# Kernel optimization log

Hardware: AMD Instinct MI355X
Metric: run time of the kernel (lower is better)

The kernel has to match this reference:

```python
import jax, jax.numpy as jnp
import numpy as np

N = 100_000      # total nodes across batch of graphs
E = 1_600_000    # total directed edges
D = 128          # input feature dim
H = 128          # hidden dim
OUT = 10         # output classes
B = 500          # number of graphs (200 nodes each)
L_MID = 3        # GIN layers after the first (num_layers-2)


def setup_inputs() -> dict:
    key = jax.random.key(0)
    ks = jax.random.split(key, 24)
    s = np.float32(1.0 / np.sqrt(H))
    f32 = jnp.float32
    inp = {
        'node_features': jax.random.normal(ks[0], (N, D), f32),
        'edge_src': jax.random.randint(ks[1], (E,), 0, N, jnp.int32),
        'edge_dst': jax.random.randint(ks[2], (E,), 0, N, jnp.int32),
        'graph_ids': (jnp.arange(N) // (N // B)).astype(jnp.int32),
        # GIN eps per layer (torch init: zeros)
        'eps': jnp.zeros((4,), f32),
        # pre MLP (input layer): Linear(D,H) -> BN -> ReLU -> Linear(H,H), then pre_batchnorm
        'pre_W1': jax.random.normal(ks[3], (D, H), f32) * s,
        'pre_b1': jnp.zeros((H,), f32),
        'pre_g1': jnp.ones((H,), f32),
        'pre_bt1': jnp.zeros((H,), f32),
        'pre_W2': jax.random.normal(ks[4], (H, H), f32) * s,
        'pre_b2': jnp.zeros((H,), f32),
        'pre_gout': jnp.ones((H,), f32),
        'pre_btout': jnp.zeros((H,), f32),
        # middle GIN layers (stacked over L_MID)
        'mlp_W1': jax.random.normal(ks[5], (L_MID, H, H), f32) * s,
        'mlp_b1': jnp.zeros((L_MID, H), f32),
        'mlp_g1': jnp.ones((L_MID, H), f32),
        'mlp_bt1': jnp.zeros((L_MID, H), f32),
        'mlp_W2': jax.random.normal(ks[6], (L_MID, H, H), f32) * s,
        'mlp_b2': jnp.zeros((L_MID, H), f32),
        'bn_g': jnp.ones((L_MID, H), f32),
        'bn_bt': jnp.zeros((L_MID, H), f32),
        # per-layer prediction heads
        'pred_W0': jax.random.normal(ks[7], (D, OUT), f32) * s,
        'pred_b0': jnp.zeros((OUT,), f32),
        'pred_W': jax.random.normal(ks[8], (4, H, OUT), f32) * s,
        'pred_b': jnp.zeros((4, OUT), f32),
    }
    return inp


def _mlp_bn(x, W1, b1, g1, bt1, W2, b2, go, bo):
    # MLP(num_mlp_layers=2): Linear -> BN(eval) -> ReLU -> Linear, then outer BN(eval) -> ReLU
    h = jax.nn.relu(g1 * (x @ W1 + b1) + bt1)
    h = h @ W2 + b2
    return jax.nn.relu(go * h + bo)


def reference(node_features, edge_src, edge_dst, graph_ids, eps,
              pre_W1, pre_b1, pre_g1, pre_bt1, pre_W2, pre_b2, pre_gout, pre_btout,
              mlp_W1, mlp_b1, mlp_g1, mlp_bt1, mlp_W2, mlp_b2, bn_g, bn_bt,
              pred_W0, pred_b0, pred_W, pred_b):
    def agg(h):
        # sparse Adj @ h via gather + segment_sum (sum neighbor pooling, learn_eps=True -> no self loops)
        return jax.ops.segment_sum(h[edge_src], edge_dst, num_segments=N)

    h = node_features
    reps = [h]
    pooled = agg(h) + (1.0 + eps[0]) * h
    h = _mlp_bn(pooled, pre_W1, pre_b1, pre_g1, pre_bt1, pre_W2, pre_b2, pre_gout, pre_btout)
    reps.append(h)
    for i in range(L_MID):
        pooled = agg(h) + (1.0 + eps[i + 1]) * h
        h = _mlp_bn(pooled, mlp_W1[i], mlp_b1[i], mlp_g1[i], mlp_bt1[i],
                    mlp_W2[i], mlp_b2[i], bn_g[i], bn_bt[i])
        reps.append(h)

    # graph-level sum pooling + per-layer linear heads (dropout off in eval)
    score = jax.ops.segment_sum(reps[0], graph_ids, num_segments=B) @ pred_W0 + pred_b0
    for k in range(4):
        score = score + jax.ops.segment_sum(reps[k + 1], graph_ids, num_segments=B) @ pred_W[k] + pred_b[k]
    return score  # [B, OUT]
```

## Files before the change

### kernel.cpp

```cpp
#include <hip/hip_runtime.h>
#include <hip/hip_bf16.h>

#define NN 100000
#define EE 1600000
#define HH 128
#define OUTC 10
#define BB 500
#define GSZ 200
#define LDA 136

#define NBKT 782
#define BCAP 2560
#define EPB 4096
#define NTILE64 1563

typedef float f32x4 __attribute__((ext_vector_type(4)));
typedef __bf16 bf16x8 __attribute__((ext_vector_type(8)));

__device__ __forceinline__ float b2f(unsigned short u){
    unsigned int x = ((unsigned int)u) << 16;
    return __builtin_bit_cast(float, x);
}
__device__ __forceinline__ unsigned short f2b(float f){
    __hip_bfloat16 h = __float2bfloat16(f);
    return __builtin_bit_cast(unsigned short, h);
}

__global__ __launch_bounds__(256) void k_bucket(const int* __restrict__ src, const int* __restrict__ dst,
                                                int* __restrict__ bucket_cursor, unsigned int* __restrict__ ebuf){
    __shared__ unsigned int val[EPB];
    __shared__ unsigned short bkt[EPB];
    __shared__ int hist[NBKT];
    int t = threadIdx.x;
    int e0 = blockIdx.x * EPB;
    for (int i = t; i < NBKT; i += 256) hist[i] = 0;
    __syncthreads();
    for (int i = t; i < EPB; i += 256){
        int e = e0 + i;
        if (e < EE){
            int d = dst[e];
            int b = d >> 7;
            val[i] = ((unsigned)src[e] << 7) | (unsigned)(d & 127);
            bkt[i] = (unsigned short)b;
            atomicAdd(&hist[b], 1);
        } else {
            bkt[i] = 0xffff;
        }
    }
    __syncthreads();
    for (int i = t; i < NBKT; i += 256){
        int c = hist[i];
        hist[i] = c ? atomicAdd(&bucket_cursor[i], c) : 0;
    }
    __syncthreads();
    for (int i = t; i < EPB; i += 256){
        unsigned short b = bkt[i];
        if (b != 0xffff){
            int pos = atomicAdd(&hist[b], 1);
            if (pos < BCAP) ebuf[(int)b * BCAP + pos] = val[i];
        }
    }
}

__global__ __launch_bounds__(1024) void k_bscan(const int* __restrict__ bucket_cursor,
                                                int* __restrict__ bucket_base, int* __restrict__ row_ptr){
    __shared__ int tmp[1024];
    int t = threadIdx.x;
    int v = (t < NBKT) ? min(bucket_cursor[t], BCAP) : 0;
    tmp[t] = v; __syncthreads();
    for (int off = 1; off < 1024; off <<= 1){
        int a = (t >= off) ? tmp[t - off] : 0;
        __syncthreads();
        tmp[t] += a;
        __syncthreads();
    }
    if (t < NBKT) bucket_base[t + 1] = tmp[t];
    if (t == 0){ bucket_base[0] = 0; row_ptr[NN] = EE; }
}

__global__ __launch_bounds__(256) void k_csr(const int* __restrict__ bucket_cursor, const int* __restrict__ bucket_base,
                                             const unsigned int* __restrict__ ebuf,
                                             int* __restrict__ row_ptr, int* __restrict__ col){
    __shared__ int cnt[128];
    __shared__ int pfx[128];
    int b = blockIdx.x;
    int t = threadIdx.x;
    int c    = min(bucket_cursor[b], BCAP);
    int base = bucket_base[b];
    if (t < 128) cnt[t] = 0;
    __syncthreads();
    const unsigned int* eb = ebuf + (size_t)b * BCAP;
    for (int i = t; i < c; i += 256) atomicAdd(&cnt[eb[i] & 127], 1);
    __syncthreads();
    if (t == 0){
        int run = 0;
        for (int i = 0; i < 128; ++i){ pfx[i] = run; run += cnt[i]; }
    }
    __syncthreads();
    int node0 = b * 128;
    if (t < 128 && node0 + t < NN) row_ptr[node0 + t] = base + pfx[t];
    if (t < 128) cnt[t] = pfx[t];
    __syncthreads();
    for (int i = t; i < c; i += 256){
        unsigned int v = eb[i];
        int pos = atomicAdd(&cnt[v & 127], 1);
        col[base + pos] = (int)(v >> 7);
    }
}

__global__ __launch_bounds__(256) void k_prep(const float* __restrict__ preW1, const float* __restrict__ preW2,
                                              const float* __restrict__ mlpW1, const float* __restrict__ mlpW2,
                                              unsigned short* __restrict__ Wbf){
    int idx = blockIdx.x*256 + threadIdx.x;
    int w = idx >> 14;
    int rem = idx & 16383;
    int e = rem & 7;
    int chunk = rem >> 3;
    int m = chunk & 15;
    int q = (chunk >> 4) & 3;
    int kk = (chunk >> 6) & 3;
    int j = chunk >> 8;
    int n = j*16 + m;
    int k = kk*32 + q*8 + e;
    const float* src;
    if      (w == 0) src = preW1;
    else if (w == 1) src = preW2;
    else if (w <  5) src = mlpW1 + (w-2)*16384;
    else             src = mlpW2 + (w-5)*16384;
    Wbf[idx] = f2b(src[k*128 + n]);
}

__global__ __launch_bounds__(256) void k_input(const float* __restrict__ x, unsigned short* __restrict__ hA,
                                               float* __restrict__ G){
    __shared__ float r0[256], r1[256];
    int t = threadIdx.x;
    int f2 = t & 63;
    int rg = t >> 6;
    int g  = blockIdx.x;
    if (t < 128){
        #pragma unroll
        for (int k = 1; k < 5; ++k) G[(size_t)k*BB*128 + g*128 + t] = 0.f;
    }
    float a0 = 0.f, a1 = 0.f;
    for (int i = rg; i < GSZ; i += 4){
        int node = g*GSZ + i;
        float2 v = *(const float2*)(x + (size_t)node*128 + f2*2);
        a0 += v.x; a1 += v.y;
        unsigned int o = (unsigned)f2b(v.x) | ((unsigned)f2b(v.y) << 16);
        ((unsigned int*)hA)[(size_t)node*64 + f2] = o;
    }
    r0[t] = a0; r1[t] = a1;
    __syncthreads();
    if (t < 64){
        float s0 = r0[t] + r0[t+64] + r0[t+128] + r0[t+192];
        float s1 = r1[t] + r1[t+64] + r1[t+128] + r1[t+192];
        float2 v; v.x = s0; v.y = s1;
        *(float2*)(G + g*128 + t*2) = v;
    }
}

__device__ __forceinline__ void acc_u32(float* a, unsigned int v, int j){
    a[j]   += __builtin_bit_cast(float, v << 16);
    a[j+1] += __builtin_bit_cast(float, v & 0xffff0000u);
}
__device__ __forceinline__ void acc_u4(float* a, uint4 v){
    acc_u32(a, v.x, 0); acc_u32(a, v.y, 2); acc_u32(a, v.z, 4); acc_u32(a, v.w, 6);
}

__global__ __launch_bounds__(256) void k_agg(const int* __restrict__ row_ptr, const int* __restrict__ col,
                                             const unsigned short* __restrict__ h,
                                             const float* __restrict__ eps, int l,
                                             unsigned short* __restrict__ pooled){
    int lane = threadIdx.x & 63;
    int wv   = threadIdx.x >> 6;
    int n    = blockIdx.x*4 + wv;
    int q = lane >> 4;
    int u = lane & 15;
    int beg = row_ptr[n], end = row_ptr[n+1];
    float a[8];
    #pragma unroll
    for (int j = 0; j < 8; ++j) a[j] = 0.f;

    int e = beg;
    for (; e + 16 <= end; e += 16){
        int c0 = col[e      + q];
        int c1 = col[e + 4  + q];
        int c2 = col[e + 8  + q];
        int c3 = col[e + 12 + q];
        uint4 v0 = *(const uint4*)(h + (size_t)c0*128 + u*8);
        uint4 v1 = *(const uint4*)(h + (size_t)c1*128 + u*8);
        uint4 v2 = *(const uint4*)(h + (size_t)c2*128 + u*8);
        uint4 v3 = *(const uint4*)(h + (size_t)c3*128 + u*8);
        acc_u4(a, v0); acc_u4(a, v1); acc_u4(a, v2); acc_u4(a, v3);
    }
    for (; e + 4 <= end; e += 4){
        int c = col[e + q];
        uint4 v = *(const uint4*)(h + (size_t)c*128 + u*8);
        acc_u4(a, v);
    }
    if (e < end){
        if (e + q < end){
            int c = col[e + q];
            uint4 v = *(const uint4*)(h + (size_t)c*128 + u*8);
            acc_u4(a, v);
        }
    }
    #pragma unroll
    for (int j = 0; j < 8; ++j){
        a[j] += __shfl_xor(a[j], 16, 64);
        a[j] += __shfl_xor(a[j], 32, 64);
    }
    if (q == 0){
        float ep = 1.0f + eps[l];
        uint4 hs = *(const uint4*)(h + (size_t)n*128 + u*8);
        a[0] += ep * __builtin_bit_cast(float, hs.x << 16);
        a[1] += ep * __builtin_bit_cast(float, hs.x & 0xffff0000u);
        a[2] += ep * __builtin_bit_cast(float, hs.y << 16);
        a[3] += ep * __builtin_bit_cast(float, hs.y & 0xffff0000u);
        a[4] += ep * __builtin_bit_cast(float, hs.z << 16);
        a[5] += ep * __builtin_bit_cast(float, hs.z & 0xffff0000u);
        a[6] += ep * __builtin_bit_cast(float, hs.w << 16);
        a[7] += ep * __builtin_bit_cast(float, hs.w & 0xffff0000u);
        uint4 o;
        o.x = (unsigned)f2b(a[0]) | ((unsigned)f2b(a[1]) << 16);
        o.y = (unsigned)f2b(a[2]) | ((unsigned)f2b(a[3]) << 16);
        o.z = (unsigned)f2b(a[4]) | ((unsigned)f2b(a[5]) << 16);
        o.w = (unsigned)f2b(a[6]) | ((unsigned)f2b(a[7]) << 16);
        *(uint4*)(pooled + (size_t)n*128 + u*8) = o;
    }
}

__global__ __launch_bounds__(256, 4) void k_mlp1(const unsigned short* __restrict__ Ain,
                                                 unsigned short* __restrict__ Yout,
                                                 const unsigned short* __restrict__ Wf,
                                                 const float* __restrict__ bb, const float* __restrict__ gg,
                                                 const float* __restrict__ bt){
    __shared__ __align__(16) unsigned short Wl[16384];
    __shared__ __align__(16) unsigned short Ys[4][16*LDA];
    int t = threadIdx.x;
    int lane = t & 63, wv = t >> 6;
    int m = lane & 15, q = lane >> 4;
    for (int i = t; i < 2048; i += 256)
        *(int4*)(&Wl[i*8]) = *(const int4*)(Wf + i*8);
    __syncthreads();
    float ge[8], ce[8];
    #pragma unroll
    for (int j = 0; j < 8; ++j){
        int colc = j*16 + m;
        float gv = gg[colc];
        ge[j] = gv; ce[j] = bb[colc]*gv + bt[colc];
    }
    unsigned short* Y = &Ys[wv][0];
    for (int tile = blockIdx.x; tile < NTILE64; tile += gridDim.x){
        int row0 = tile*64 + wv*16;
        int node = row0 + m;
        bool valid = node < NN;
        size_t nb = (size_t)(valid ? node : 0) * 128;
        bf16x8 a[4];
        #pragma unroll
        for (int kk = 0; kk < 4; ++kk){
            int4 v = *(const int4*)(Ain + nb + kk*32 + q*8);
            if (!valid) v = make_int4(0,0,0,0);
            a[kk] = __builtin_bit_cast(bf16x8, v);
        }
        f32x4 acc[8];
        #pragma unroll
        for (int j = 0; j < 8; ++j) acc[j] = (f32x4){0.f,0.f,0.f,0.f};
        #pragma unroll
        for (int kk = 0; kk < 4; ++kk){
            #pragma unroll
            for (int j = 0; j < 8; ++j){
                bf16x8 b = *(const bf16x8*)(&Wl[((((j*4+kk)*4+q)*16)+m)*8]);
                acc[j] = __builtin_amdgcn_mfma_f32_16x16x32_bf16(a[kk], b, acc[j], 0, 0, 0);
            }
        }
        #pragma unroll
        for (int j = 0; j < 8; ++j){
            int colc = j*16 + m;
            #pragma unroll
            for (int r = 0; r < 4; ++r){
                float v = fmaxf(acc[j][r]*ge[j] + ce[j], 0.f);
                Y[(q*4 + r)*LDA + colc] = f2b(v);
            }
        }
        #pragma unroll
        for (int i = 0; i < 4; ++i){
            int idx = i*64 + lane;
            int r = idx >> 4, c = idx & 15;
            int nd = tile*64 + wv*16 + r;
            if (nd < NN)
                *(int4*)(Yout + (size_t)nd*128 + c*8) = *(const int4*)(&Y[r*LDA + c*8]);
        }
    }
}

__global__ __launch_bounds__(256, 4) void k_mlp2(const unsigned short* __restrict__ Ain,
                                                 unsigned short* __restrict__ Out,
                                                 const unsigned short* __restrict__ Wf,
                                                 const float* __restrict__ bb, const float* __restrict__ gg,
                                                 const float* __restrict__ bt,
                                                 float* __restrict__ Gout){
    __shared__ __align__(16) unsigned short Wl[16384];
    __shared__ __align__(16) unsigned short Ys[4][16*LDA];
    int t = threadIdx.x;
    int lane = t & 63, wv = t >> 6;
    int m = lane & 15, q = lane >> 4;
    for (int i = t; i < 2048; i += 256)
        *(int4*)(&Wl[i*8]) = *(const int4*)(Wf + i*8);
    __syncthreads();
    float ge[8], ce[8];
    #pragma unroll
    for (int j = 0; j < 8; ++j){
        int colc = j*16 + m;
        float gv = gg[colc];
        ge[j] = gv; ce[j] = bb[colc]*gv + bt[colc];
    }
    unsigned short* Y = &Ys[wv][0];
    for (int tile = blockIdx.x; tile < NTILE64; tile += gridDim.x){
        int row0 = tile*64 + wv*16;
        int node = row0 + m;
        bool valid = node < NN;
        size_t nb = (size_t)(valid ? node : 0) * 128;
        bf16x8 a[4];
        #pragma unroll
        for (int kk = 0; kk < 4; ++kk){
            int4 v = *(const int4*)(Ain + nb + kk*32 + q*8);
            if (!valid) v = make_int4(0,0,0,0);
            a[kk] = __builtin_bit_cast(bf16x8, v);
        }
        f32x4 acc[8];
        #pragma unroll
        for (int j = 0; j < 8; ++j) acc[j] = (f32x4){0.f,0.f,0.f,0.f};
        #pragma unroll
        for (int kk = 0; kk < 4; ++kk){
            #pragma unroll
            for (int j = 0; j < 8; ++j){
                bf16x8 b = *(const bf16x8*)(&Wl[((((j*4+kk)*4+q)*16)+m)*8]);
                acc[j] = __builtin_amdgcn_mfma_f32_16x16x32_bf16(a[kk], b, acc[j], 0, 0, 0);
            }
        }
        #pragma unroll
        for (int j = 0; j < 8; ++j){
            int colc = j*16 + m;
            #pragma unroll
            for (int r = 0; r < 4; ++r){
                float v = fmaxf(acc[j][r]*ge[j] + ce[j], 0.f);
                Y[(q*4 + r)*LDA + colc] = f2b(v);
            }
        }
        #pragma unroll
        for (int i = 0; i < 4; ++i){
            int idx = i*64 + lane;
            int r = idx >> 4, c = idx & 15;
            int nd = tile*64 + wv*16 + r;
            if (nd < NN)
                *(int4*)(Out + (size_t)nd*128 + c*8) = *(const int4*)(&Y[r*LDA + c*8]);
        }
        {
            float run0 = 0.f, run1 = 0.f;
            int curg = row0 / GSZ;
            for (int r = 0; r < 16; ++r){
                int nd = row0 + r;
                if (nd >= NN) break;
                int g = nd / GSZ;
                if (g != curg){
                    if (run0 != 0.f) atomicAdd(&Gout[curg*128 + lane], run0);
                    if (run1 != 0.f) atomicAdd(&Gout[curg*128 + lane + 64], run1);
                    run0 = 0.f; run1 = 0.f; curg = g;
                }
                run0 += b2f(Y[r*LDA + lane]);
                run1 += b2f(Y[r*LDA + lane + 64]);
            }
            if (run0 != 0.f) atomicAdd(&Gout[curg*128 + lane], run0);
            if (run1 != 0.f) atomicAdd(&Gout[curg*128 + lane + 64], run1);
        }
    }
}

__global__ __launch_bounds__(256) void k_score(const float* __restrict__ G,
                                               const float* __restrict__ W0, const float* __restrict__ b0,
                                               const float* __restrict__ Wk, const float* __restrict__ bk,
                                               float* __restrict__ out){
    int id = blockIdx.x*256 + threadIdx.x;
    if (id >= BB*OUTC) return;
    int b = id / OUTC, o = id % OUTC;
    float s = b0[o];
    #pragma unroll
    for (int k = 0; k < 4; ++k) s += bk[k*OUTC + o];
    const float* g0 = G + b*128;
    for (int c = 0; c < 128; ++c) s += g0[c] * W0[c*OUTC + o];
    for (int k = 0; k < 4; ++k){
        const float* gk = G + (size_t)(k+1)*BB*128 + b*128;
        const float* wk = Wk + k*128*OUTC;
        for (int c = 0; c < 128; ++c) s += gk[c] * wk[c*OUTC + o];
    }
    out[id] = s;
}

extern "C" void kernel_launch(void* const* d_in, const int* in_sizes, int n_in,
                              void* d_out, int out_size, void* d_ws, size_t ws_size,
                              hipStream_t stream){
    const float* node_features = (const float*)d_in[0];
    const int*   edge_src  = (const int*)d_in[1];
    const int*   edge_dst  = (const int*)d_in[2];
    const float* eps       = (const float*)d_in[4];
    const float* pre_W1    = (const float*)d_in[5];
    const float* pre_b1    = (const float*)d_in[6];
    const float* pre_g1    = (const float*)d_in[7];
    const float* pre_bt1   = (const float*)d_in[8];
    const float* pre_W2    = (const float*)d_in[9];
    const float* pre_b2    = (const float*)d_in[10];
    const float* pre_gout  = (const float*)d_in[11];
    const float* pre_btout = (const float*)d_in[12];
    const float* mlp_W1    = (const float*)d_in[13];
    const float* mlp_b1    = (const float*)d_in[14];
    const float* mlp_g1    = (const float*)d_in[15];
    const float* mlp_bt1   = (const float*)d_in[16];
    const float* mlp_W2    = (const float*)d_in[17];
    const float* mlp_b2    = (const float*)d_in[18];
    const float* bn_g      = (const float*)d_in[19];
    const float* bn_bt     = (const float*)d_in[20];
    const float* pred_W0   = (const float*)d_in[21];
    const float* pred_b0   = (const float*)d_in[22];
    const float* pred_W    = (const float*)d_in[23];
    const float* pred_b    = (const float*)d_in[24];
    float* out = (float*)d_out;

    char* p = (char*)d_ws;
    auto alloc = [&](size_t bytes)->char*{
        char* r = p;
        p += (bytes + 255) & ~(size_t)255;
        return r;
    };
    int* bucket_cursor    = (int*)alloc((size_t)NBKT*4);
    int* bucket_base      = (int*)alloc((size_t)(NBKT+1)*4);
    int* row_ptr          = (int*)alloc((size_t)(NN+1)*4);
    int* col              = (int*)alloc((size_t)EE*4);
    unsigned int* ebuf    = (unsigned int*)alloc((size_t)NBKT*BCAP*4);
    unsigned short* Wbf   = (unsigned short*)alloc((size_t)8*128*128*2);
    unsigned short* hA    = (unsigned short*)alloc((size_t)NN*128*2);
    unsigned short* hB    = (unsigned short*)alloc((size_t)NN*128*2);
    unsigned short* pooled= (unsigned short*)alloc((size_t)NN*128*2);
    float* G              = (float*)alloc((size_t)5*BB*128*4);

    hipMemsetAsync(bucket_cursor, 0, (size_t)NBKT*4, stream);

    k_bucket<<<(EE + EPB - 1)/EPB, 256, 0, stream>>>(edge_src, edge_dst, bucket_cursor, ebuf);
    k_bscan<<<1, 1024, 0, stream>>>(bucket_cursor, bucket_base, row_ptr);
    k_csr<<<NBKT, 256, 0, stream>>>(bucket_cursor, bucket_base, ebuf, row_ptr, col);

    k_input<<<BB, 256, 0, stream>>>(node_features, hA, G);
    k_prep<<<512, 256, 0, stream>>>(pre_W1, pre_W2, mlp_W1, mlp_W2, Wbf);

    const unsigned short* hcur = hA;
    unsigned short* hnxt = hB;
    for (int l = 0; l < 4; ++l){
        k_agg<<<NN/4, 256, 0, stream>>>(row_ptr, col, hcur, eps, l, pooled);
        const unsigned short *W1t, *W2t;
        const float *b1,*g1,*bt1,*b2,*g2,*bt2;
        if (l == 0){
            W1t = Wbf;             W2t = Wbf + 16384;
            b1 = pre_b1; g1 = pre_g1; bt1 = pre_bt1;
            b2 = pre_b2; g2 = pre_gout; bt2 = pre_btout;
        } else {
            W1t = Wbf + (size_t)(2 + (l-1))*16384;
            W2t = Wbf + (size_t)(5 + (l-1))*16384;
            b1 = mlp_b1 + (l-1)*128; g1 = mlp_g1 + (l-1)*128; bt1 = mlp_bt1 + (l-1)*128;
            b2 = mlp_b2 + (l-1)*128; g2 = bn_g   + (l-1)*128; bt2 = bn_bt   + (l-1)*128;
        }
        k_mlp1<<<768, 256, 0, stream>>>(pooled, pooled, W1t, b1, g1, bt1);
        k_mlp2<<<768, 256, 0, stream>>>(pooled, hnxt, W2t, b2, g2, bt2,
                                        G + (size_t)(l+1)*BB*128);
        const unsigned short* tmp = hnxt;
        hnxt = (unsigned short*)hcur;
        hcur = tmp;
    }
    k_score<<<(BB*OUTC + 255)/256, 256, 0, stream>>>(G, pred_W0, pred_b0, pred_W, pred_b, out);
}
```

Measured before the change: 636.3 us.

## Merge setup kernels, prefetch next MLP tile, branchless agg tail, paired pooling reads

Combines the edge bucketing, input conversion and weight prep kernels into one launch dispatched by block index, removing two launches and letting the independent phases overlap. The MLP kernels now prefetch the next tile's A fragment into registers while computing the current one, which uses more registers. The aggregation tail is replaced by one masked 16-edge step with clamped indices instead of a loop plus a remainder branch. The graph pooling reads two adjacent bf16 values per lane and changes which columns each lane accumulates.

```diff
diff --git a/kernel.cpp b/kernel.cpp
--- a/kernel.cpp
+++ b/kernel.cpp
@@ -12,6 +12,7 @@
 #define NBKT 782
 #define BCAP 2560
 #define EPB 4096
+#define NBUCKB 391
 #define NTILE64 1563
 
 typedef float f32x4 __attribute__((ext_vector_type(4)));
@@ -26,39 +27,92 @@
     return __builtin_bit_cast(unsigned short, h);
 }
 
-__global__ __launch_bounds__(256) void k_bucket(const int* __restrict__ src, const int* __restrict__ dst,
-                                                int* __restrict__ bucket_cursor, unsigned int* __restrict__ ebuf){
-    __shared__ unsigned int val[EPB];
-    __shared__ unsigned short bkt[EPB];
-    __shared__ int hist[NBKT];
+__global__ __launch_bounds__(256) void k_setup(const int* __restrict__ src, const int* __restrict__ dst,
+                                               int* __restrict__ bucket_cursor, unsigned int* __restrict__ ebuf,
+                                               const float* __restrict__ x, unsigned short* __restrict__ hA,
+                                               float* __restrict__ G,
+                                               const float* __restrict__ preW1, const float* __restrict__ preW2,
+                                               const float* __restrict__ mlpW1, const float* __restrict__ mlpW2,
+                                               unsigned short* __restrict__ Wbf){
+    __shared__ __align__(16) unsigned int sval[EPB];
+    __shared__ unsigned short sbkt[EPB];
+    __shared__ int shist[NBKT];
     int t = threadIdx.x;
-    int e0 = blockIdx.x * EPB;
-    for (int i = t; i < NBKT; i += 256) hist[i] = 0;
-    __syncthreads();
-    for (int i = t; i < EPB; i += 256){
-        int e = e0 + i;
-        if (e < EE){
-            int d = dst[e];
-            int b = d >> 7;
-            val[i] = ((unsigned)src[e] << 7) | (unsigned)(d & 127);
-            bkt[i] = (unsigned short)b;
-            atomicAdd(&hist[b], 1);
-        } else {
-            bkt[i] = 0xffff;
-        }
-    }
-    __syncthreads();
-    for (int i = t; i < NBKT; i += 256){
-        int c = hist[i];
-        hist[i] = c ? atomicAdd(&bucket_cursor[i], c) : 0;
-    }
-    __syncthreads();
-    for (int i = t; i < EPB; i += 256){
-        unsigned short b = bkt[i];
-        if (b != 0xffff){
-            int pos = atomicAdd(&hist[b], 1);
-            if (pos < BCAP) ebuf[(int)b * BCAP + pos] = val[i];
-        }
+    int bid = blockIdx.x;
+
+    if (bid < NBUCKB){
+        int e0 = bid * EPB;
+        for (int i = t; i < NBKT; i += 256) shist[i] = 0;
+        __syncthreads();
+        for (int i = t; i < EPB; i += 256){
+            int e = e0 + i;
+            if (e < EE){
+                int d = dst[e];
+                int b = d >> 7;
+                sval[i] = ((unsigned)src[e] << 7) | (unsigned)(d & 127);
+                sbkt[i] = (unsigned short)b;
+                atomicAdd(&shist[b], 1);
+            } else {
+                sbkt[i] = 0xffff;
+            }
+        }
+        __syncthreads();
+        for (int i = t; i < NBKT; i += 256){
+            int c = shist[i];
+            shist[i] = c ? atomicAdd(&bucket_cursor[i], c) : 0;
+        }
+        __syncthreads();
+        for (int i = t; i < EPB; i += 256){
+            unsigned short b = sbkt[i];
+            if (b != 0xffff){
+                int pos = atomicAdd(&shist[b], 1);
+                if (pos < BCAP) ebuf[(int)b * BCAP + pos] = sval[i];
+            }
+        }
+    } else if (bid < NBUCKB + BB){
+        float* r0 = (float*)sval;
+        float* r1 = r0 + 256;
+        int g = bid - NBUCKB;
+        int f2 = t & 63;
+        int rg = t >> 6;
+        if (t < 128){
+            #pragma unroll
+            for (int k = 1; k < 5; ++k) G[(size_t)k*BB*128 + g*128 + t] = 0.f;
+        }
+        float a0 = 0.f, a1 = 0.f;
+        for (int i = rg; i < GSZ; i += 4){
+            int node = g*GSZ + i;
+            float2 v = *(const float2*)(x + (size_t)node*128 + f2*2);
+            a0 += v.x; a1 += v.y;
+            unsigned int o = (unsigned)f2b(v.x) | ((unsigned)f2b(v.y) << 16);
+            ((unsigned int*)hA)[(size_t)node*64 + f2] = o;
+        }
+        r0[t] = a0; r1[t] = a1;
+        __syncthreads();
+        if (t < 64){
+            float s0 = r0[t] + r0[t+64] + r0[t+128] + r0[t+192];
+            float s1 = r1[t] + r1[t+64] + r1[t+128] + r1[t+192];
+            float2 v; v.x = s0; v.y = s1;
+            *(float2*)(G + g*128 + t*2) = v;
+        }
+    } else {
+        int idx = (bid - NBUCKB - BB)*256 + t;
+        int w = idx >> 14;
+        int rem = idx & 16383;
+        int e = rem & 7;
+        int chunk = rem >> 3;
+        int m = chunk & 15;
+        int q = (chunk >> 4) & 3;
+        int kk = (chunk >> 6) & 3;
+        int j = chunk >> 8;
+        int n = j*16 + m;
+        int k = kk*32 + q*8 + e;
+        const float* s;
+        if      (w == 0) s = preW1;
+        else if (w == 1) s = preW2;
+        else if (w <  5) s = mlpW1 + (w-2)*16384;
+        else             s = mlpW2 + (w-5)*16384;
+        Wbf[idx] = f2b(s[k*128 + n]);
     }
 }
 
@@ -108,63 +162,15 @@
     }
 }
 
-__global__ __launch_bounds__(256) void k_prep(const float* __restrict__ preW1, const float* __restrict__ preW2,
-                                              const float* __restrict__ mlpW1, const float* __restrict__ mlpW2,
-                                              unsigned short* __restrict__ Wbf){
-    int idx = blockIdx.x*256 + threadIdx.x;
-    int w = idx >> 14;
-    int rem = idx & 16383;
-    int e = rem & 7;
-    int chunk = rem >> 3;
-    int m = chunk & 15;
-    int q = (chunk >> 4) & 3;
-    int kk = (chunk >> 6) & 3;
-    int j = chunk >> 8;
-    int n = j*16 + m;
-    int k = kk*32 + q*8 + e;
-    const float* src;
-    if      (w == 0) src = preW1;
-    else if (w == 1) src = preW2;
-    else if (w <  5) src = mlpW1 + (w-2)*16384;
-    else             src = mlpW2 + (w-5)*16384;
-    Wbf[idx] = f2b(src[k*128 + n]);
-}
-
-__global__ __launch_bounds__(256) void k_input(const float* __restrict__ x, unsigned short* __restrict__ hA,
-                                               float* __restrict__ G){
-    __shared__ float r0[256], r1[256];
-    int t = threadIdx.x;
-    int f2 = t & 63;
-    int rg = t >> 6;
-    int g  = blockIdx.x;
-    if (t < 128){
-        #pragma unroll
-        for (int k = 1; k < 5; ++k) G[(size_t)k*BB*128 + g*128 + t] = 0.f;
-    }
-    float a0 = 0.f, a1 = 0.f;
-    for (int i = rg; i < GSZ; i += 4){
-        int node = g*GSZ + i;
-        float2 v = *(const float2*)(x + (size_t)node*128 + f2*2);
-        a0 += v.x; a1 += v.y;
-        unsigned int o = (unsigned)f2b(v.x) | ((unsigned)f2b(v.y) << 16);
-        ((unsigned int*)hA)[(size_t)node*64 + f2] = o;
-    }
-    r0[t] = a0; r1[t] = a1;
-    __syncthreads();
-    if (t < 64){
-        float s0 = r0[t] + r0[t+64] + r0[t+128] + r0[t+192];
-        float s1 = r1[t] + r1[t+64] + r1[t+128] + r1[t+192];
-        float2 v; v.x = s0; v.y = s1;
-        *(float2*)(G + g*128 + t*2) = v;
-    }
-}
-
 __device__ __forceinline__ void acc_u32(float* a, unsigned int v, int j){
     a[j]   += __builtin_bit_cast(float, v << 16);
     a[j+1] += __builtin_bit_cast(float, v & 0xffff0000u);
 }
 __device__ __forceinline__ void acc_u4(float* a, uint4 v){
     acc_u32(a, v.x, 0); acc_u32(a, v.y, 2); acc_u32(a, v.z, 4); acc_u32(a, v.w, 6);
+}
+__device__ __forceinline__ uint4 and4(uint4 v, unsigned mk){
+    v.x &= mk; v.y &= mk; v.z &= mk; v.w &= mk; return v;
 }
 
 __global__ __launch_bounds__(256) void k_agg(const int* __restrict__ row_ptr, const int* __restrict__ col,
@@ -193,17 +199,22 @@
         uint4 v3 = *(const uint4*)(h + (size_t)c3*128 + u*8);
         acc_u4(a, v0); acc_u4(a, v1); acc_u4(a, v2); acc_u4(a, v3);
     }
-    for (; e + 4 <= end; e += 4){
-        int c = col[e + q];
-        uint4 v = *(const uint4*)(h + (size_t)c*128 + u*8);
-        acc_u4(a, v);
-    }
     if (e < end){
-        if (e + q < end){
-            int c = col[e + q];
-            uint4 v = *(const uint4*)(h + (size_t)c*128 + u*8);
-            acc_u4(a, v);
-        }
+        int last = end - 1;
+        int i0 = e + q, i1 = e + 4 + q, i2 = e + 8 + q, i3 = e + 12 + q;
+        int c0 = col[min(i0, last)];
+        int c1 = col[min(i1, last)];
+        int c2 = col[min(i2, last)];
+        int c3 = col[min(i3, last)];
+        uint4 v0 = *(const uint4*)(h + (size_t)c0*128 + u*8);
+        uint4 v1 = *(const uint4*)(h + (size_t)c1*128 + u*8);
+        uint4 v2 = *(const uint4*)(h + (size_t)c2*128 + u*8);
+        uint4 v3 = *(const uint4*)(h + (size_t)c3*128 + u*8);
+        v0 = and4(v0, (i0 < end) ? 0xffffffffu : 0u);
+        v1 = and4(v1, (i1 < end) ? 0xffffffffu : 0u);
+        v2 = and4(v2, (i2 < end) ? 0xffffffffu : 0u);
+        v3 = and4(v3, (i3 < end) ? 0xffffffffu : 0u);
+        acc_u4(a, v0); acc_u4(a, v1); acc_u4(a, v2); acc_u4(a, v3);
     }
     #pragma unroll
     for (int j = 0; j < 8; ++j){
@@ -227,6 +238,19 @@
         o.z = (unsigned)f2b(a[4]) | ((unsigned)f2b(a[5]) << 16);
         o.w = (unsigned)f2b(a[6]) | ((unsigned)f2b(a[7]) << 16);
         *(uint4*)(pooled + (size_t)n*128 + u*8) = o;
+    }
+}
+
+__device__ __forceinline__ void load_a(const unsigned short* __restrict__ Ain, int tile,
+                                       int wv, int m, int q, bf16x8* dst){
+    int node = tile*64 + wv*16 + m;
+    bool valid = node < NN;
+    const unsigned short* base = Ain + (size_t)(valid ? node : 0)*128 + q*8;
+    #pragma unroll
+    for (int kk = 0; kk < 4; ++kk){
+        int4 v = *(const int4*)(base + kk*32);
+        if (!valid) v = make_int4(0,0,0,0);
+        dst[kk] = __builtin_bit_cast(bf16x8, v);
     }
 }
 
@@ -251,18 +275,15 @@
         ge[j] = gv; ce[j] = bb[colc]*gv + bt[colc];
     }
     unsigned short* Y = &Ys[wv][0];
-    for (int tile = blockIdx.x; tile < NTILE64; tile += gridDim.x){
-        int row0 = tile*64 + wv*16;
-        int node = row0 + m;
-        bool valid = node < NN;
-        size_t nb = (size_t)(valid ? node : 0) * 128;
+    int tile = blockIdx.x;
+    bf16x8 aN[4];
+    if (tile < NTILE64) load_a(Ain, tile, wv, m, q, aN);
+    while (tile < NTILE64){
         bf16x8 a[4];
         #pragma unroll
-        for (int kk = 0; kk < 4; ++kk){
-            int4 v = *(const int4*)(Ain + nb + kk*32 + q*8);
-            if (!valid) v = make_int4(0,0,0,0);
-            a[kk] = __builtin_bit_cast(bf16x8, v);
-        }
+        for (int kk = 0; kk < 4; ++kk) a[kk] = aN[kk];
+        int nxt = tile + gridDim.x;
+        if (nxt < NTILE64) load_a(Ain, nxt, wv, m, q, aN);
         f32x4 acc[8];
         #pragma unroll
         for (int j = 0; j < 8; ++j) acc[j] = (f32x4){0.f,0.f,0.f,0.f};
@@ -291,6 +312,7 @@
             if (nd < NN)
                 *(int4*)(Yout + (size_t)nd*128 + c*8) = *(const int4*)(&Y[r*LDA + c*8]);
         }
+        tile = nxt;
     }
 }
 
@@ -316,18 +338,15 @@
         ge[j] = gv; ce[j] = bb[colc]*gv + bt[colc];
     }
     unsigned short* Y = &Ys[wv][0];
-    for (int tile = blockIdx.x; tile < NTILE64; tile += gridDim.x){
-        int row0 = tile*64 + wv*16;
-        int node = row0 + m;
-        bool valid = node < NN;
-        size_t nb = (size_t)(valid ? node : 0) * 128;
+    int tile = blockIdx.x;
+    bf16x8 aN[4];
+    if (tile < NTILE64) load_a(Ain, tile, wv, m, q, aN);
+    while (tile < NTILE64){
         bf16x8 a[4];
         #pragma unroll
-        for (int kk = 0; kk < 4; ++kk){
-            int4 v = *(const int4*)(Ain + nb + kk*32 + q*8);
-            if (!valid) v = make_int4(0,0,0,0);
-            a[kk] = __builtin_bit_cast(bf16x8, v);
-        }
+        for (int kk = 0; kk < 4; ++kk) a[kk] = aN[kk];
+        int nxt = tile + gridDim.x;
+        if (nxt < NTILE64) load_a(Ain, nxt, wv, m, q, aN);
         f32x4 acc[8];
         #pragma unroll
         for (int j = 0; j < 8; ++j) acc[j] = (f32x4){0.f,0.f,0.f,0.f};
@@ -348,11 +367,12 @@
                 Y[(q*4 + r)*LDA + colc] = f2b(v);
             }
         }
+        int row0 = tile*64 + wv*16;
         #pragma unroll
         for (int i = 0; i < 4; ++i){
             int idx = i*64 + lane;
             int r = idx >> 4, c = idx & 15;
-            int nd = tile*64 + wv*16 + r;
+            int nd = row0 + r;
             if (nd < NN)
                 *(int4*)(Out + (size_t)nd*128 + c*8) = *(const int4*)(&Y[r*LDA + c*8]);
         }
@@ -364,16 +384,18 @@
                 if (nd >= NN) break;
                 int g = nd / GSZ;
                 if (g != curg){
-                    if (run0 != 0.f) atomicAdd(&Gout[curg*128 + lane], run0);
-                    if (run1 != 0.f) atomicAdd(&Gout[curg*128 + lane + 64], run1);
+                    if (run0 != 0.f) atomicAdd(&Gout[curg*128 + lane*2], run0);
+                    if (run1 != 0.f) atomicAdd(&Gout[curg*128 + lane*2 + 1], run1);
                     run0 = 0.f; run1 = 0.f; curg = g;
                 }
-                run0 += b2f(Y[r*LDA + lane]);
-                run1 += b2f(Y[r*LDA + lane + 64]);
-            }
-            if (run0 != 0.f) atomicAdd(&Gout[curg*128 + lane], run0);
-            if (run1 != 0.f) atomicAdd(&Gout[curg*128 + lane + 64], run1);
-        }
+                unsigned int v = *(const unsigned int*)(&Y[r*LDA + lane*2]);
+                run0 += b2f((unsigned short)v);
+                run1 += b2f((unsigned short)(v >> 16));
+            }
+            if (run0 != 0.f) atomicAdd(&Gout[curg*128 + lane*2], run0);
+            if (run1 != 0.f) atomicAdd(&Gout[curg*128 + lane*2 + 1], run1);
+        }
+        tile = nxt;
     }
 }
 
@@ -445,12 +467,11 @@
 
     hipMemsetAsync(bucket_cursor, 0, (size_t)NBKT*4, stream);
 
-    k_bucket<<<(EE + EPB - 1)/EPB, 256, 0, stream>>>(edge_src, edge_dst, bucket_cursor, ebuf);
+    k_setup<<<NBUCKB + BB + 512, 256, 0, stream>>>(edge_src, edge_dst, bucket_cursor, ebuf,
+                                                   node_features, hA, G,
+                                                   pre_W1, pre_W2, mlp_W1, mlp_W2, Wbf);
     k_bscan<<<1, 1024, 0, stream>>>(bucket_cursor, bucket_base, row_ptr);
     k_csr<<<NBKT, 256, 0, stream>>>(bucket_cursor, bucket_base, ebuf, row_ptr, col);
-
-    k_input<<<BB, 256, 0, stream>>>(node_features, hA, G);
-    k_prep<<<512, 256, 0, stream>>>(pre_W1, pre_W2, mlp_W1, mlp_W2, Wbf);
 
     const unsigned short* hcur = hA;
     unsigned short* hnxt = hB;
```

After: 609.3 us (median of 2 runs). 1.04x faster.
